# Performance work log

Hardware: AMD Instinct MI355X
Metric: run time of the kernel (lower is better)

## Reference

```python
import jax, jax.numpy as jnp
import numpy as np

N_NODES = 50000
N_EDGES = 800000
IN_DIM_N = 256
IN_DIM_E = 64
OUT_DIM_N = 64
OUT_DIM_E = 64


def setup_inputs() -> dict:
    key = jax.random.key(0)
    ks = jax.random.split(key, 8)
    nfeats = jax.random.normal(ks[0], (N_NODES, IN_DIM_N), dtype=jnp.float32)
    efeats = jax.random.normal(ks[1], (N_EDGES, IN_DIM_E), dtype=jnp.float32)
    src = jax.random.randint(ks[2], (N_EDGES,), 0, N_NODES)
    dst = jax.random.randint(ks[3], (N_EDGES,), 0, N_NODES)
    # xavier-style scaled weights
    W_fc = jax.random.normal(ks[4], (OUT_DIM_N, IN_DIM_N), dtype=jnp.float32) * (2.0 / (OUT_DIM_N + IN_DIM_N)) ** 0.5
    cat_dim = IN_DIM_E + 2 * OUT_DIM_N  # 192
    W_e = jax.random.normal(ks[5], (OUT_DIM_E, cat_dim), dtype=jnp.float32) * (2.0 / (OUT_DIM_E + cat_dim)) ** 0.5
    b_e = jnp.zeros((OUT_DIM_E,), dtype=jnp.float32)
    w_c = jax.random.normal(ks[6], (1, OUT_DIM_E), dtype=jnp.float32) * (2.0 / (1 + OUT_DIM_E)) ** 0.5
    return {"nfeats": nfeats, "efeats": efeats, "src": src, "dst": dst,
            "W_fc": W_fc, "W_e": W_e, "b_e": b_e, "w_c": w_c}


def reference(nfeats, efeats, src, dst, W_fc, W_e, b_e, w_c):
    N = nfeats.shape[0]
    # node projection (no bias)
    z = nfeats @ W_fc.T                                   # [N, out_n]
    # edge attention MLP on [z_src | efeat | z_dst]
    stacked = jnp.concatenate([z[src], efeats, z[dst]], axis=1)  # [E, in_e + 2*out_n]
    feat_e = jax.nn.leaky_relu(stacked @ W_e.T + b_e)     # [E, out_e], slope 0.01 = torch default
    a = (feat_e @ w_c.T)[:, 0]                            # [E]
    # segment softmax over incoming edges of each dst node
    m = jax.ops.segment_max(a, dst, num_segments=N)       # [N] (-inf for empty segs, never gathered)
    ex = jnp.exp(a - m[dst])                              # [E]
    s = jax.ops.segment_sum(ex, dst, num_segments=N)      # [N]
    alpha = ex / s[dst]                                   # [E]
    # weighted scatter-sum aggregate of source z
    h = jax.ops.segment_sum(alpha[:, None] * z[src], dst, num_segments=N)  # [N, out_n]
    return h, feat_e
```

## Files before the change

### kernel.cpp

```cpp
#include <hip/hip_runtime.h>
#include <hip/hip_bf16.h>

#define N_NODES 50000
#define N_EDGES 800000
#define IN_N    256
#define D       64

typedef __attribute__((ext_vector_type(8))) short short8;
typedef __attribute__((ext_vector_type(4))) float f32x4;

__device__ __forceinline__ float bf2f(unsigned short h) {
    union { unsigned int u; float f; } x; x.u = ((unsigned int)h) << 16; return x.f;
}
__device__ __forceinline__ unsigned short f2bf(float f) {
    union { float f; unsigned int u; } x; x.f = f;
    unsigned int r = x.u + 0x7fff + ((x.u >> 16) & 1);
    return (unsigned short)(r >> 16);
}
__device__ __forceinline__ short8 pack8(f32x4 p0, f32x4 p1) {
    short8 r;
    r[0] = (short)f2bf(p0[0]); r[1] = (short)f2bf(p0[1]);
    r[2] = (short)f2bf(p0[2]); r[3] = (short)f2bf(p0[3]);
    r[4] = (short)f2bf(p1[0]); r[5] = (short)f2bf(p1[1]);
    r[6] = (short)f2bf(p1[2]); r[7] = (short)f2bf(p1[3]);
    return r;
}

__global__ void zero_kernel(f32x4* __restrict__ p, int n4) {
    int i = blockIdx.x * blockDim.x + threadIdx.x;
    int stride = gridDim.x * blockDim.x;
    f32x4 z = {0.f, 0.f, 0.f, 0.f};
    for (; i < n4; i += stride) p[i] = z;
}

__global__ __launch_bounds__(256) void proj_kernel(
    const float* __restrict__ nf, const float* __restrict__ W_fc,
    unsigned short* __restrict__ z_bf)
{
    __shared__ unsigned short wl[64 * 264];
    for (int i = threadIdx.x; i < 64 * 256; i += 256)
        wl[(i >> 8) * 264 + (i & 255)] = f2bf(W_fc[i]);
    __syncthreads();
    const int lanelo = threadIdx.x & 15, quad = (threadIdx.x >> 4) & 3;
    const int wflat = blockIdx.x * 4 + (threadIdx.x >> 6);
    const int nw = gridDim.x * 4;
    const f32x4 z4 = {0.f, 0.f, 0.f, 0.f};
    for (int g = wflat; g < N_NODES / 16; g += nw) {
        const int n0 = g * 16;
        f32x4 acc[4] = {z4, z4, z4, z4};
        const float* arow = nf + (size_t)(n0 + lanelo) * IN_N;
        #pragma unroll
        for (int h = 0; h < 8; ++h) {
            const float* ap = arow + h * 32 + quad * 8;
            f32x4 p0 = *(const f32x4*)ap;
            f32x4 p1 = *(const f32x4*)(ap + 4);
            short8 a = pack8(p0, p1);
            #pragma unroll
            for (int t = 0; t < 4; ++t) {
                short8 b = *(const short8*)&wl[(t * 16 + lanelo) * 264 + h * 32 + quad * 8];
                acc[t] = __builtin_amdgcn_mfma_f32_16x16x32_bf16(a, b, acc[t], 0, 0, 0);
            }
        }
        #pragma unroll
        for (int t = 0; t < 4; ++t)
            #pragma unroll
            for (int r = 0; r < 4; ++r)
                z_bf[(size_t)(n0 + quad * 4 + r) * D + t * 16 + lanelo] = f2bf(acc[t][r]);
    }
}

__global__ __launch_bounds__(256) void uv_kernel(
    const unsigned short* __restrict__ z_bf, const float* __restrict__ W_e,
    const float* __restrict__ b_e,
    unsigned short* __restrict__ u_bf, unsigned short* __restrict__ v_bf)
{
    __shared__ unsigned short wl[128 * 72];
    for (int i = threadIdx.x; i < 128 * 64; i += 256) {
        int row = i >> 6, col = i & 63;
        float val = (row < 64) ? W_e[(size_t)row * 192 + col]
                               : W_e[(size_t)(row - 64) * 192 + 128 + col];
        wl[row * 72 + col] = f2bf(val);
    }
    __syncthreads();
    const int lanelo = threadIdx.x & 15, quad = (threadIdx.x >> 4) & 3;
    float bias[4];
    #pragma unroll
    for (int t = 0; t < 4; ++t) bias[t] = b_e[t * 16 + lanelo];
    const int wflat = blockIdx.x * 4 + (threadIdx.x >> 6);
    const int nw = gridDim.x * 4;
    const f32x4 z4 = {0.f, 0.f, 0.f, 0.f};
    for (int g = wflat; g < N_NODES / 16; g += nw) {
        const int n0 = g * 16;
        f32x4 acc[8] = {z4, z4, z4, z4, z4, z4, z4, z4};
        #pragma unroll
        for (int h = 0; h < 2; ++h) {
            short8 a = *(const short8*)(z_bf + (size_t)(n0 + lanelo) * D + h * 32 + quad * 8);
            #pragma unroll
            for (int t = 0; t < 8; ++t) {
                short8 b = *(const short8*)&wl[(t * 16 + lanelo) * 72 + h * 32 + quad * 8];
                acc[t] = __builtin_amdgcn_mfma_f32_16x16x32_bf16(a, b, acc[t], 0, 0, 0);
            }
        }
        #pragma unroll
        for (int t = 0; t < 4; ++t)
            #pragma unroll
            for (int r = 0; r < 4; ++r)
                u_bf[(size_t)(n0 + quad * 4 + r) * D + t * 16 + lanelo] = f2bf(acc[t][r] + bias[t]);
        #pragma unroll
        for (int t = 4; t < 8; ++t)
            #pragma unroll
            for (int r = 0; r < 4; ++r)
                v_bf[(size_t)(n0 + quad * 4 + r) * D + (t - 4) * 16 + lanelo] = f2bf(acc[t][r]);
    }
}

__global__ __launch_bounds__(256) void edge_kernel(
    const float* __restrict__ efeats,
    const int* __restrict__ src, const int* __restrict__ dst,
    const float* __restrict__ W_e, const float* __restrict__ w_c,
    const unsigned short* __restrict__ u_bf, const unsigned short* __restrict__ v_bf,
    const unsigned short* __restrict__ z_bf,
    float* __restrict__ s, float* __restrict__ num,
    float* __restrict__ feat_out)
{
    const int lanelo = threadIdx.x & 15, quad = (threadIdx.x >> 4) & 3;
    short8 b2[4][2];
    #pragma unroll
    for (int t = 0; t < 4; ++t)
        #pragma unroll
        for (int h = 0; h < 2; ++h)
            #pragma unroll
            for (int j = 0; j < 8; ++j)
                b2[t][h][j] = (short)f2bf(W_e[(size_t)(t * 16 + lanelo) * 192 + 64 + h * 32 + quad * 8 + j]);
    float wcv[4];
    #pragma unroll
    for (int t = 0; t < 4; ++t) wcv[t] = w_c[t * 16 + lanelo];

    const int wflat = blockIdx.x * 4 + (threadIdx.x >> 6);
    const int nw = gridDim.x * 4;
    const f32x4 z4 = {0.f, 0.f, 0.f, 0.f};
    for (int g = wflat; g < N_EDGES / 16; g += nw) {
        const int e0 = g * 16;
        f32x4 acc[4] = {z4, z4, z4, z4};
        const float* ar = efeats + (size_t)(e0 + lanelo) * D;
        #pragma unroll
        for (int h = 0; h < 2; ++h) {
            f32x4 p0 = *(const f32x4*)(ar + h * 32 + quad * 8);
            f32x4 p1 = *(const f32x4*)(ar + h * 32 + quad * 8 + 4);
            short8 a = pack8(p0, p1);
            #pragma unroll
            for (int t = 0; t < 4; ++t)
                acc[t] = __builtin_amdgcn_mfma_f32_16x16x32_bf16(a, b2[t][h], acc[t], 0, 0, 0);
        }
        int sn[4], dn[4];
        #pragma unroll
        for (int r = 0; r < 4; ++r) {
            sn[r] = src[e0 + quad * 4 + r];
            dn[r] = dst[e0 + quad * 4 + r];
        }
        float part[4];
        #pragma unroll
        for (int r = 0; r < 4; ++r) {
            float p = 0.f;
            #pragma unroll
            for (int t = 0; t < 4; ++t) {
                float f = acc[t][r]
                        + bf2f(u_bf[(size_t)sn[r] * D + t * 16 + lanelo])
                        + bf2f(v_bf[(size_t)dn[r] * D + t * 16 + lanelo]);
                f = f > 0.f ? f : 0.01f * f;
                feat_out[(size_t)(e0 + quad * 4 + r) * D + t * 16 + lanelo] = f;
                p += f * wcv[t];
            }
            part[r] = p;
        }
        #pragma unroll
        for (int st = 1; st < 16; st <<= 1) {
            #pragma unroll
            for (int r = 0; r < 4; ++r) part[r] += __shfl_xor(part[r], st, 64);
        }
        #pragma unroll
        for (int r = 0; r < 4; ++r) {
            float ex = __expf(part[r]);
            #pragma unroll
            for (int t = 0; t < 4; ++t) {
                float zz = bf2f(z_bf[(size_t)sn[r] * D + t * 16 + lanelo]);
                atomicAdd(&num[(size_t)dn[r] * D + t * 16 + lanelo], ex * zz);
            }
            if (lanelo == 0) atomicAdd(&s[dn[r]], ex);
        }
    }
}

__global__ void final_kernel(const float* __restrict__ num,
                             const float* __restrict__ s,
                             float* __restrict__ h)
{
    int i = blockIdx.x * blockDim.x + threadIdx.x;
    if (i < N_NODES * D) {
        float sv = s[i >> 6];
        h[i] = sv > 0.f ? num[i] / sv : 0.f;
    }
}

extern "C" void kernel_launch(void* const* d_in, const int* in_sizes, int n_in,
                              void* d_out, int out_size, void* d_ws, size_t ws_size,
                              hipStream_t stream)
{
    const float* nfeats = (const float*)d_in[0];
    const float* efeats = (const float*)d_in[1];
    const int* src = (const int*)d_in[2];
    const int* dst = (const int*)d_in[3];
    const float* W_fc = (const float*)d_in[4];
    const float* W_e  = (const float*)d_in[5];
    const float* b_e  = (const float*)d_in[6];
    const float* w_c  = (const float*)d_in[7];

    unsigned short* z_bf = (unsigned short*)d_ws;
    unsigned short* u_bf = z_bf + (size_t)N_NODES * D;
    unsigned short* v_bf = u_bf + (size_t)N_NODES * D;
    float* s   = (float*)(v_bf + (size_t)N_NODES * D);
    float* num = s + N_NODES;

    float* h_out = (float*)d_out;
    float* f_out = h_out + (size_t)N_NODES * D;

    zero_kernel<<<1024, 256, 0, stream>>>((f32x4*)s, (N_NODES + N_NODES * D) / 4);
    proj_kernel<<<782, 256, 0, stream>>>(nfeats, W_fc, z_bf);
    uv_kernel<<<782, 256, 0, stream>>>(z_bf, W_e, b_e, u_bf, v_bf);
    edge_kernel<<<2048, 256, 0, stream>>>(efeats, src, dst, W_e, w_c, u_bf, v_bf, z_bf, s, num, f_out);
    final_kernel<<<12500, 256, 0, stream>>>(num, s, h_out);
}
```

Baseline: 633.7 us.

## Replace per-edge float atomics with CSR bucketing and per-node gather aggregation

Builds a dst-sorted CSR on each call: count in-degrees, scan them to offsets, then have the edge kernel append (exp score, src) pairs into per-destination buckets through an atomic cursor. A new aggregation kernel gives each node one wavefront that gathers z rows and does the weighted sum and normalisation, replacing the 64 float atomics per edge and the separate finalize pass. The cost is extra kernels (a single-block scan, a count pass), a scattered 8-byte write per edge, and a non-deterministic ordering of terms within each node's sum.

```diff
diff --git a/kernel.cpp b/kernel.cpp
--- a/kernel.cpp
+++ b/kernel.cpp
@@ -26,11 +26,54 @@
     return r;
 }
 
-__global__ void zero_kernel(f32x4* __restrict__ p, int n4) {
+__global__ void zero_int_kernel(int* __restrict__ p, int n) {
     int i = blockIdx.x * blockDim.x + threadIdx.x;
     int stride = gridDim.x * blockDim.x;
-    f32x4 z = {0.f, 0.f, 0.f, 0.f};
-    for (; i < n4; i += stride) p[i] = z;
+    for (; i < n; i += stride) p[i] = 0;
+}
+
+__global__ void count_kernel(const int* __restrict__ dst, int* __restrict__ count) {
+    int i = blockIdx.x * blockDim.x + threadIdx.x;
+    int stride = gridDim.x * blockDim.x;
+    for (; i < N_EDGES / 4; i += stride) {
+        int4 d = ((const int4*)dst)[i];
+        atomicAdd(&count[d.x], 1);
+        atomicAdd(&count[d.y], 1);
+        atomicAdd(&count[d.z], 1);
+        atomicAdd(&count[d.w], 1);
+    }
+}
+
+__global__ __launch_bounds__(1024) void scan_kernel(const int* __restrict__ count,
+                                                    int* __restrict__ offsets,
+                                                    int* __restrict__ cursor) {
+    __shared__ int part[1024];
+    const int t = threadIdx.x;
+    const int C = (N_NODES + 1023) / 1024;
+    const int base = t * C;
+    int s = 0;
+    for (int i = 0; i < C; ++i) {
+        int idx = base + i;
+        if (idx < N_NODES) s += count[idx];
+    }
+    part[t] = s;
+    __syncthreads();
+    for (int st = 1; st < 1024; st <<= 1) {
+        int v = (t >= st) ? part[t - st] : 0;
+        __syncthreads();
+        part[t] += v;
+        __syncthreads();
+    }
+    int run = part[t] - s;
+    for (int i = 0; i < C; ++i) {
+        int idx = base + i;
+        if (idx < N_NODES) {
+            offsets[idx] = run;
+            cursor[idx]  = run;
+            run += count[idx];
+        }
+    }
+    if (t == 1023) offsets[N_NODES] = part[1023];
 }
 
 __global__ __launch_bounds__(256) void proj_kernel(
@@ -119,8 +162,7 @@
     const int* __restrict__ src, const int* __restrict__ dst,
     const float* __restrict__ W_e, const float* __restrict__ w_c,
     const unsigned short* __restrict__ u_bf, const unsigned short* __restrict__ v_bf,
-    const unsigned short* __restrict__ z_bf,
-    float* __restrict__ s, float* __restrict__ num,
+    int* __restrict__ cursor, unsigned long long* __restrict__ csr,
     float* __restrict__ feat_out)
 {
     const int lanelo = threadIdx.x & 15, quad = (threadIdx.x >> 4) & 3;
@@ -181,24 +223,50 @@
         #pragma unroll
         for (int r = 0; r < 4; ++r) {
             float ex = __expf(part[r]);
-            #pragma unroll
-            for (int t = 0; t < 4; ++t) {
-                float zz = bf2f(z_bf[(size_t)sn[r] * D + t * 16 + lanelo]);
-                atomicAdd(&num[(size_t)dn[r] * D + t * 16 + lanelo], ex * zz);
+            if (lanelo == 0) {
+                int pos = atomicAdd(&cursor[dn[r]], 1);
+                csr[pos] = ((unsigned long long)__float_as_uint(ex) << 32)
+                         | (unsigned long long)(unsigned int)sn[r];
             }
-            if (lanelo == 0) atomicAdd(&s[dn[r]], ex);
-        }
-    }
-}
-
-__global__ void final_kernel(const float* __restrict__ num,
-                             const float* __restrict__ s,
-                             float* __restrict__ h)
-{
-    int i = blockIdx.x * blockDim.x + threadIdx.x;
-    if (i < N_NODES * D) {
-        float sv = s[i >> 6];
-        h[i] = sv > 0.f ? num[i] / sv : 0.f;
+        }
+    }
+}
+
+__global__ __launch_bounds__(256) void agg_kernel(
+    const unsigned long long* __restrict__ csr,
+    const int* __restrict__ offsets,
+    const unsigned short* __restrict__ z_bf,
+    float* __restrict__ h)
+{
+    const int lane = threadIdx.x & 63;
+    const int wid = (blockIdx.x * blockDim.x + threadIdx.x) >> 6;
+    const int nw = (gridDim.x * blockDim.x) >> 6;
+    for (int n = wid; n < N_NODES; n += nw) {
+        const int off = offsets[n];
+        const int end = offsets[n + 1];
+        float acc = 0.f, ssum = 0.f;
+        int e = off;
+        for (; e + 1 < end; e += 2) {
+            unsigned long long p0 = csr[e];
+            unsigned long long p1 = csr[e + 1];
+            float x0 = __uint_as_float((unsigned int)(p0 >> 32));
+            float x1 = __uint_as_float((unsigned int)(p1 >> 32));
+            int s0 = (int)(p0 & 0xffffffffu);
+            int s1 = (int)(p1 & 0xffffffffu);
+            float z0 = bf2f(z_bf[(size_t)s0 * D + lane]);
+            float z1 = bf2f(z_bf[(size_t)s1 * D + lane]);
+            acc += x0 * z0;
+            acc += x1 * z1;
+            ssum += x0 + x1;
+        }
+        if (e < end) {
+            unsigned long long p0 = csr[e];
+            float x0 = __uint_as_float((unsigned int)(p0 >> 32));
+            int s0 = (int)(p0 & 0xffffffffu);
+            acc += x0 * bf2f(z_bf[(size_t)s0 * D + lane]);
+            ssum += x0;
+        }
+        h[(size_t)n * D + lane] = ssum > 0.f ? acc / ssum : 0.f;
     }
 }
 
@@ -218,15 +286,20 @@
     unsigned short* z_bf = (unsigned short*)d_ws;
     unsigned short* u_bf = z_bf + (size_t)N_NODES * D;
     unsigned short* v_bf = u_bf + (size_t)N_NODES * D;
-    float* s   = (float*)(v_bf + (size_t)N_NODES * D);
-    float* num = s + N_NODES;
+    unsigned long long* csr = (unsigned long long*)(v_bf + (size_t)N_NODES * D);
+    int* count   = (int*)(csr + (size_t)N_EDGES);
+    int* offsets = count + N_NODES;
+    int* cursor  = offsets + N_NODES + 1;
 
     float* h_out = (float*)d_out;
     float* f_out = h_out + (size_t)N_NODES * D;
 
-    zero_kernel<<<1024, 256, 0, stream>>>((f32x4*)s, (N_NODES + N_NODES * D) / 4);
+    zero_int_kernel<<<64, 256, 0, stream>>>(count, N_NODES);
+    count_kernel<<<512, 256, 0, stream>>>(dst, count);
+    scan_kernel<<<1, 1024, 0, stream>>>(count, offsets, cursor);
     proj_kernel<<<782, 256, 0, stream>>>(nfeats, W_fc, z_bf);
     uv_kernel<<<782, 256, 0, stream>>>(z_bf, W_e, b_e, u_bf, v_bf);
-    edge_kernel<<<2048, 256, 0, stream>>>(efeats, src, dst, W_e, w_c, u_bf, v_bf, z_bf, s, num, f_out);
-    final_kernel<<<12500, 256, 0, stream>>>(num, s, h_out);
-}
+    edge_kernel<<<2048, 256, 0, stream>>>(efeats, src, dst, W_e, w_c, u_bf, v_bf,
+                                          cursor, csr, f_out);
+    agg_kernel<<<2048, 256, 0, stream>>>(csr, offsets, z_bf, h_out);
+}
```

New measurement: 709.3 us. 1.12x slower.
